# Kernel optimization log

Hardware: AMD Instinct MI355X
Metric: run time of the kernel (lower is better)

Reference implementation:

```python
import jax, jax.numpy as jnp
import numpy as np
from math import factorial, sqrt

# ---------------- irreps utilities ----------------
def parse(s):
    out = []
    for tok in s.split('+'):
        tok = tok.strip()
        mul, ir = (tok.split('x') if 'x' in tok else ('1', tok))
        out.append((int(mul), int(ir[:-1]), 1 if ir[-1] == 'e' else -1))
    return out

def irdim(ir):
    return sum(m * (2 * l + 1) for m, l, p in ir)

def slices(ir):
    s, o = [], 0
    for m, l, p in ir:
        s.append((o, m, l, p)); o += m * (2 * l + 1)
    return s

# ---------------- real Clebsch-Gordan coefficients ----------------
def _cgc(j1, m1, j2, m2, j3, m3):
    if m1 + m2 != m3:
        return 0.0
    f = factorial
    pre = sqrt((2 * j3 + 1) * f(j3 + j1 - j2) * f(j3 - j1 + j2) * f(j1 + j2 - j3) / f(j1 + j2 + j3 + 1))
    pre *= sqrt(f(j3 + m3) * f(j3 - m3) * f(j1 - m1) * f(j1 + m1) * f(j2 - m2) * f(j2 + m2))
    s = 0.0
    for k in range(max(0, j2 - j3 - m1, j1 - j3 + m2), min(j1 + j2 - j3, j1 - m1, j2 + m2) + 1):
        s += (-1) ** k / (f(k) * f(j1 + j2 - j3 - k) * f(j1 - m1 - k) * f(j2 + m2 - k) * f(j3 - j2 + m1 + k) * f(j3 - j1 - m2 + k))
    return pre * s

def _c2r(l):
    # complex -> real spherical-harmonic change of basis
    q = np.zeros((2 * l + 1, 2 * l + 1), dtype=complex); r2 = 1 / np.sqrt(2)
    q[l, l] = 1.0
    for mu in range(1, l + 1):
        q[mu + l, mu + l] = (-1) ** mu * r2; q[mu + l, -mu + l] = r2
        q[-mu + l, -mu + l] = 1j * r2;       q[-mu + l, mu + l] = -1j * (-1) ** mu * r2
    return q

_CGMEM = {}
def cg_real(l1, l2, l3):
    key = (l1, l2, l3)
    if key in _CGMEM:
        return _CGMEM[key]
    C = np.zeros((2 * l1 + 1, 2 * l2 + 1, 2 * l3 + 1))
    for m1 in range(-l1, l1 + 1):
        for m2 in range(-l2, l2 + 1):
            if abs(m1 + m2) <= l3:
                C[m1 + l1, m2 + l2, m1 + m2 + l3] = _cgc(l1, m1, l2, m2, l3, m1 + m2)
    T = np.einsum('am,bn,co,mno->abc', _c2r(l1), _c2r(l2), np.conj(_c2r(l3)), C)
    R = T.real if np.abs(T.real).sum() >= np.abs(T.imag).sum() else T.imag
    _CGMEM[key] = np.ascontiguousarray(R)
    return _CGMEM[key]

# ---------------- equivariant ops ----------------
def tp_paths(ir1, ir2, iro):
    P = []
    for (o1, m1, l1, p1) in slices(ir1):
        for (o2, m2, l2, p2) in slices(ir2):
            for (oo, mo, lo, po) in slices(iro):
                if po == p1 * p2 and abs(l1 - l2) <= lo <= l1 + l2:
                    P.append((o1, m1, l1, o2, m2, l2, oo, mo, lo))
    return P

def tp_numel(P):
    return sum(m1 * m2 * mo for (_, m1, _, _, m2, _, _, mo, _) in P)

def tp_apply(ir1, ir2, iro, x1, x2, w):
    # FullyConnectedTensorProduct with per-row (shared_weights=False) weights w:[E, numel]
    P = tp_paths(ir1, ir2, iro)
    out = jnp.zeros((x1.shape[0], irdim(iro)), x1.dtype)
    fan = {}
    for p in P:
        fan[p[6]] = fan.get(p[6], 0) + p[1] * p[4]
    off = 0
    for (o1, m1, l1, o2, m2, l2, oo, mo, lo) in P:
        cg = jnp.asarray(cg_real(l1, l2, lo), x1.dtype)
        a = x1[:, o1:o1 + m1 * (2 * l1 + 1)].reshape(-1, m1, 2 * l1 + 1)
        b = x2[:, o2:o2 + m2 * (2 * l2 + 1)].reshape(-1, m2, 2 * l2 + 1)
        ww = w[:, off:off + m1 * m2 * mo].reshape(-1, m1, m2, mo); off += m1 * m2 * mo
        r = jnp.einsum('eui,evj,euvw,ijk->ewk', a, b, ww, cg) / np.sqrt(fan[oo])
        out = out.at[:, oo:oo + mo * (2 * lo + 1)].add(r.reshape(-1, mo * (2 * lo + 1)))
    return out

def lin_pairs(iri, iro):
    return [(si, so) for si in slices(iri) for so in slices(iro) if si[2] == so[2] and si[3] == so[3]]

def lin_numel(iri, iro):
    return sum(si[1] * so[1] for si, so in lin_pairs(iri, iro))

def lin_apply(iri, iro, x, w):
    # o3.Linear: per-irrep channel mixing with fan-in normalization
    out = jnp.zeros((x.shape[0], irdim(iro)), x.dtype)
    pairs = lin_pairs(iri, iro)
    fan = {}
    for si, so in pairs:
        fan[so[0]] = fan.get(so[0], 0) + si[1]
    off = 0
    for (oi, mi, li, pi), (oo, mo, lo, po) in pairs:
        W = w[off:off + mi * mo].reshape(mi, mo); off += mi * mo
        xb = x[:, oi:oi + mi * (2 * li + 1)].reshape(-1, mi, 2 * li + 1)
        r = jnp.einsum('eui,uv->evi', xb, W) / np.sqrt(fan[oo])
        out = out.at[:, oo:oo + mo * (2 * lo + 1)].add(r.reshape(-1, mo * (2 * lo + 1)))
    return out

def act_apply(ir, acts, x):
    # tanh on scalar irreps only (flags in acts), identity elsewhere
    parts = []
    for (o, m, l, p), a in zip(slices(ir), acts):
        b = x[:, o:o + m * (2 * l + 1)]
        parts.append(jnp.tanh(b) if a else b)
    return jnp.concatenate(parts, axis=1)

def fc_apply(x, w, dims):
    # e3nn FullyConnectedNet: relu MLP with 1/sqrt(fan_in) weight normalization
    off, h = 0, x
    for i in range(len(dims) - 1):
        di, do = dims[i], dims[i + 1]
        W = w[off:off + di * do].reshape(di, do); off += di * do
        h = (h @ W) / np.sqrt(di)
        if i < len(dims) - 2:
            h = jax.nn.relu(h)
    return h

# ---------------- module irreps (from V_theta.__init__) ----------------
IRR_IN = parse('2x0e')
IRR_SH = parse('1x0e+1x1o+1x2e')
MID1 = parse('8x0e+8x1o+8x2e')
MID2 = parse('8x0e+8x0o+8x1e+8x1o+8x2e+8x2o')
IRR_HH = parse('4x0e+2x1o+2x1o+1x0e+1x1e+1x2e')
IRR_CC = parse('9x0e+6x1o+3x2e+6x1o+' + '1x0e+1x1e+1x2e+' * 4 + '1x1o+1x2o+1x3o+' * 2 + '3x2e+' + '1x1o+1x2o+1x3o+' * 2 + '1x0e+1x1e+1x2e+1x3e+1x4e')
IRR_CH = parse('6x0e+3x1o+4x1o+' + '1x0e+1x1e+1x2e+' * 2 + '2x2e+1x1o+1x2o+1x3o')
SCR = parse('32x0e+1x2e'); SCR2 = parse('1x0e+1x2e'); G1 = parse('32x0e'); G2 = parse('3x0e')
ACT2 = [1, 0, 0]; ACT3 = [1, 1, 0, 0, 0, 0]
P1 = tp_paths(IRR_IN, IRR_SH, MID1); P2 = tp_paths(MID1, IRR_SH, MID2); PB = tp_paths(MID2, MID2, MID2)
EMB_N = 16
FC1D = [1, EMB_N, EMB_N, EMB_N, tp_numel(P1)]
FC2D = [1, EMB_N, EMB_N, EMB_N, tp_numel(P2)]
FCBD = [1, EMB_N, EMB_N, EMB_N, tp_numel(PB)]

def fcsz(d):
    return sum(d[i] * d[i + 1] for i in range(len(d) - 1))

N_NODES, N_EDGES, N_BOND, SCALING = 10000, 100000, 1000, 0.2


def setup_inputs() -> dict:
    key = jax.random.key(0)
    ks = jax.random.split(key, 32)
    nrm = lambda i, shp: jax.random.normal(ks[i], shp, jnp.float32)
    return {
        'f_in': nrm(0, (N_NODES, 2)),
        'sh': nrm(1, (N_EDGES, 9)),
        'emb': jax.random.uniform(ks[2], (N_EDGES, 1), jnp.float32),
        'num_neighbors': jnp.full((1,), 10.0, jnp.float32),
        'w_lin1': nrm(3, (lin_numel(IRR_IN, IRR_IN),)),
        'w_lin2': nrm(4, (lin_numel(MID1, MID1),)),
        'w_lin3': nrm(5, (lin_numel(MID2, MID2),)),
        'w_linCC': nrm(6, (lin_numel(MID2, IRR_CC),)),
        'w_linHH': nrm(7, (lin_numel(MID2, IRR_HH),)),
        'w_linCH': nrm(8, (lin_numel(MID2, IRR_CH),)),
        'w_linC': nrm(9, (lin_numel(MID2, IRR_CC),)),
        'w_linH': nrm(10, (lin_numel(MID2, IRR_HH),)),
        'w_screen1': nrm(11, (lin_numel(MID2, SCR),)),
        'w_screen2': nrm(12, (lin_numel(SCR, SCR2),)),
        'w_gap1': nrm(13, (lin_numel(MID2, G1),)),
        'w_gap2': nrm(14, (lin_numel(G1, G2),)),
        'w_fc1': nrm(15, (fcsz(FC1D),)),
        'w_fc2': nrm(16, (fcsz(FC2D),)),
        'w_fcb': nrm(17, (fcsz(FCBD),)),
        'edge_src': jax.random.randint(ks[18], (N_EDGES,), 0, N_NODES),
        'edge_dst': jax.random.randint(ks[19], (N_EDGES,), 0, N_NODES),
        'HH_ind': jax.random.randint(ks[20], (N_BOND,), 0, N_EDGES),
        'CC_ind': jax.random.randint(ks[21], (N_BOND,), 0, N_EDGES),
        'CH_ind': jax.random.randint(ks[22], (N_BOND,), 0, N_EDGES),
        'num_nodes': N_NODES,
    }


def reference(f_in, sh, emb, num_neighbors, w_lin1, w_lin2, w_lin3, w_linCC, w_linHH, w_linCH, w_linC, w_linH, w_screen1, w_screen2, w_gap1, w_gap2, w_fc1, w_fc2, w_fcb, edge_src, edge_dst, HH_ind, CC_ind, CH_ind, num_nodes):
    inv = 1.0 / jnp.sqrt(num_neighbors)  # .div(num_neighbors**0.5)
    # layer 1: linear + tanh, gather -> TP with per-edge weights -> scatter-add
    x = jnp.tanh(lin_apply(IRR_IN, IRR_IN, f_in, w_lin1))
    ef = tp_apply(IRR_IN, IRR_SH, MID1, x[edge_src], sh, fc_apply(emb, w_fc1, FC1D))
    x = jax.ops.segment_sum(ef, edge_dst, num_segments=num_nodes) * inv
    x = act_apply(MID1, ACT2, lin_apply(MID1, MID1, x, w_lin2))
    # layer 2
    ef = tp_apply(MID1, IRR_SH, MID2, x[edge_src], sh, fc_apply(emb, w_fc2, FC2D))
    x = jax.ops.segment_sum(ef, edge_dst, num_segments=num_nodes) * inv
    x = act_apply(MID2, ACT3, lin_apply(MID2, MID2, x, w_lin3))
    # bond-level tensor products on edge subsets
    def bond(ind):
        return tp_apply(MID2, MID2, MID2, x[edge_src[ind]], x[edge_dst[ind]], fc_apply(emb[ind], w_fcb, FCBD))
    HHf, CCf, CHf = bond(HH_ind), bond(CC_ind), bond(CH_ind)
    eHH = lin_apply(MID2, IRR_HH, act_apply(MID2, ACT3, HHf), w_linHH)
    eCC = lin_apply(MID2, IRR_CC, act_apply(MID2, ACT3, CCf), w_linCC)
    eCH = lin_apply(MID2, IRR_CH, act_apply(MID2, ACT3, CHf), w_linCH)
    nC = lin_apply(MID2, IRR_CC, x, w_linC)
    nH = lin_apply(MID2, IRR_HH, x, w_linH)
    screen = lin_apply(SCR, SCR2, act_apply(SCR, [1, 0], lin_apply(MID2, SCR, x, w_screen1)), w_screen2)
    def gap(F):
        return lin_apply(G1, G2, jnp.tanh(lin_apply(MID2, G1, F, w_gap1)), w_gap2)
    s = SCALING
    # order: H, C, HH, CH, CC, screen, gap[CC], gap[HH], gap[CH]
    return (nH * s, nC * s, eHH * s, eCH * s, eCC * s, screen, gap(CCf), gap(HHf), gap(CHf))
```

## Files before the change

### kernel.cpp

```cpp
#include <hip/hip_runtime.h>
#include <hip/hip_bf16.h>

typedef __hip_bfloat16 bf16_t;

#define N_NODES 10000
#define N_EDGES 100000
#define N_BONDS 1000
#define RPW 20

__device__ __forceinline__ float bf2f(bf16_t v){ return __bfloat162float(v); }
__device__ __forceinline__ bf16_t f2bf(float v){ return __float2bfloat16(v); }
__device__ __forceinline__ int iabs(int x){ return x<0?-x:x; }

constexpr bool cg_nz(int l1,int l2,int l3,int i,int j,int k){
  int m1=i-l1, m2=j-l2, m3=k-l3;
  int neg=(m1<0)+(m2<0)+(m3<0);
  if (((neg ^ (l1+l2+l3)) & 1)!=0) return false;
  int a1=m1<0?-m1:m1, a2=m2<0?-m2:m2, a3=m3<0?-m3:m3;
  return (a3==a1+a2)||(a3==a1-a2)||(a3==a2-a1);
}

__device__ __forceinline__ void stout(void* out, size_t idx, float v, bool f32o){
  if (f32o) ((float*)out)[idx]=v;
  else      ((bf16_t*)out)[idx]=f2bf(v);
}

__global__ void detect_k(const unsigned short* nnb_raw, int* flag){
  *flag = (nnb_raw[0]==0x4120) ? 0 : 1;
}

struct CvtArgs {
  const void* src[19];
  float* dst[19];
  int n[19];
};

__global__ __launch_bounds__(256) void convert_k(CvtArgs a, const int* flag){
  bool f32 = (*flag)!=0;
  int tid = blockIdx.x*256+threadIdx.x;
  int nth = gridDim.x*256;
  for(int t=0;t<19;++t){
    int n=a.n[t];
    float* d=a.dst[t];
    if (f32){
      const float* s=(const float*)a.src[t];
      for(int i=tid;i<n;i+=nth) d[i]=s[i];
    } else {
      const bf16_t* s=(const bf16_t*)a.src[t];
      for(int i=tid;i<n;i+=nth) d[i]=bf2f(s[i]);
    }
  }
}

__global__ __launch_bounds__(256) void csr_count_k(const int* __restrict__ edst, int* __restrict__ cnt){
  int e=blockIdx.x*256+threadIdx.x; if(e>=N_EDGES) return;
  atomicAdd(&cnt[edst[e]],1);
}

__global__ __launch_bounds__(256) void csr_scan_k(const int* __restrict__ cnt,
    int* __restrict__ rowptr, int* __restrict__ pos){
  __shared__ int ssum[256];
  int t=threadIdx.x;
  int base=t*40;
  int s=0;
  for(int i=0;i<40;++i){ int idx=base+i; s += (idx<N_NODES)? cnt[idx]:0; }
  ssum[t]=s; __syncthreads();
  if(t==0){ int run=0; for(int i=0;i<256;++i){ int v=ssum[i]; ssum[i]=run; run+=v; } }
  __syncthreads();
  int run=ssum[t];
  for(int i=0;i<40;++i){
    int idx=base+i;
    if(idx<N_NODES){ rowptr[idx]=run; pos[idx]=run; run+=cnt[idx]; }
  }
  if(t==255) rowptr[N_NODES]=run;
}

__global__ __launch_bounds__(256) void csr_scatter_k(const int* __restrict__ edst,
    int* __restrict__ pos, int* __restrict__ sorted){
  int e=blockIdx.x*256+threadIdx.x; if(e>=N_EDGES) return;
  int p=atomicAdd(&pos[edst[e]],1);
  sorted[p]=e;
}

__device__ __forceinline__ double dfact(int n){
  const double F[11]={1.,1.,2.,6.,24.,120.,720.,5040.,40320.,362880.,3628800.};
  return F[n];
}

__device__ double cgc_d(int j1,int m1,int j2,int m2,int j3,int m3){
  if (m1+m2!=m3) return 0.0;
  double pre = sqrt((double)(2*j3+1)*dfact(j3+j1-j2)*dfact(j3-j1+j2)*dfact(j1+j2-j3)/dfact(j1+j2+j3+1));
  pre *= sqrt(dfact(j3+m3)*dfact(j3-m3)*dfact(j1-m1)*dfact(j1+m1)*dfact(j2-m2)*dfact(j2+m2));
  int k0 = max(0, max(j2-j3-m1, j1-j3+m2));
  int k1 = min(j1+j2-j3, min(j1-m1, j2+m2));
  double s=0.0;
  for(int k=k0;k<=k1;++k)
    s += ((k&1)?-1.0:1.0)/(dfact(k)*dfact(j1+j2-j3-k)*dfact(j1-m1-k)*dfact(j2+m2-k)*dfact(j3-j2+m1+k)*dfact(j3-j1-m2+k));
  return pre*s;
}

__device__ void c2r_d(int l,int a,int m,double&re,double&im){
  re=0.0; im=0.0;
  const double r2 = 0.7071067811865475244;
  int mu = a-l;
  if (mu==0){ if (m==l) re=1.0; return; }
  if (mu>0){
    if (m==l+mu) re = (mu&1)? -r2 : r2;
    else if (m==l-mu) re = r2;
  } else {
    int nu=-mu;
    if (m==l-nu) im = r2;
    else if (m==l+nu) im = (nu&1)? r2 : -r2;
  }
}

__global__ __launch_bounds__(128) void cg_init_k(float* cg){
  int b=blockIdx.x;
  int l1=b/9, l2=(b/3)%3, l3=b%3;
  if (l3 < iabs(l1-l2) || l3 > l1+l2) return;
  int n1=2*l1+1,n2=2*l2+1,n3=2*l3+1,n=n1*n2*n3;
  __shared__ double sRe[125], sIm[125];
  __shared__ int sPick;
  int t=threadIdx.x;
  if (t<n){
    int a=t/(n2*n3), bb=(t/n3)%n2, c=t%n3;
    double re=0.0, im=0.0;
    for(int m1=0;m1<n1;++m1){
      double q1r,q1i; c2r_d(l1,a,m1,q1r,q1i);
      if (q1r==0.0 && q1i==0.0) continue;
      for(int m2=0;m2<n2;++m2){
        double q2r,q2i; c2r_d(l2,bb,m2,q2r,q2i);
        if (q2r==0.0 && q2i==0.0) continue;
        int m3=(m1-l1)+(m2-l2)+l3;
        if (m3<0||m3>=n3) continue;
        double q3r,q3i; c2r_d(l3,c,m3,q3r,q3i); q3i=-q3i;
        double C = cgc_d(l1,m1-l1,l2,m2-l2,l3,m3-l3);
        if (C==0.0) continue;
        double ar = q1r*q2r - q1i*q2i;
        double ai = q1r*q2i + q1i*q2r;
        re += (ar*q3r - ai*q3i)*C;
        im += (ar*q3i + ai*q3r)*C;
      }
    }
    sRe[t]=re; sIm[t]=im;
  }
  __syncthreads();
  if (t==0){
    double s1=0.0,s2=0.0;
    for(int i=0;i<n;++i){ s1+=fabs(sRe[i]); s2+=fabs(sIm[i]); }
    sPick = (s1>=s2)?1:0;
  }
  __syncthreads();
  if (t<n) cg[b*125+t] = (float)(sPick? sRe[t] : sIm[t]);
}

__global__ __launch_bounds__(256) void nodeA_k(const float* __restrict__ fin,
                                               const float* __restrict__ w,
                                               float* __restrict__ x1){
  int n=blockIdx.x*256+threadIdx.x; if(n>=N_NODES) return;
  float f0=fin[2*n], f1=fin[2*n+1];
  const float r2=0.70710678f;
  x1[2*n]   = tanhf((f0*w[0]+f1*w[2])*r2);
  x1[2*n+1] = tanhf((f0*w[1]+f1*w[3])*r2);
}

__device__ __forceinline__ void mlp16(float e, const float* w, float* h){
  float a[16];
  #pragma unroll
  for(int j=0;j<16;++j) a[j]=fmaxf(e*w[j],0.f);
  float b[16];
  #pragma unroll
  for(int j=0;j<16;++j){
    float s=0.f;
    #pragma unroll
    for(int i=0;i<16;++i) s+=a[i]*w[16+i*16+j];
    b[j]=fmaxf(s*0.25f,0.f);
  }
  #pragma unroll
  for(int j=0;j<16;++j){
    float s=0.f;
    #pragma unroll
    for(int i=0;i<16;++i) s+=b[i]*w[272+i*16+j];
    h[j]=fmaxf(s*0.25f,0.f);
  }
}

__global__ __launch_bounds__(256) void hmlp_k(const float* __restrict__ emb,
    const float* __restrict__ wfc, float* __restrict__ H, int E){
  __shared__ float sw[528];
  for(int t=threadIdx.x;t<528;t+=256) sw[t]=wfc[t];
  __syncthreads();
  int e=blockIdx.x*256+threadIdx.x; if(e>=E) return;
  float h[16]; mlp16(emb[e], sw, h);
  float4* H4=(float4*)(H+(size_t)e*16);
  #pragma unroll
  for(int q=0;q<4;++q) H4[q]=make_float4(h[4*q],h[4*q+1],h[4*q+2],h[4*q+3]);
}

__global__ __launch_bounds__(256) void hb_k(const float* __restrict__ emb,
    const float* __restrict__ wfc, const int* __restrict__ i0,
    const int* __restrict__ i1, const int* __restrict__ i2,
    float* __restrict__ HB){
  __shared__ float sw[528];
  for(int t=threadIdx.x;t<528;t+=256) sw[t]=wfc[t];
  __syncthreads();
  int t=blockIdx.x*256+threadIdx.x; if(t>=3*N_BONDS) return;
  const int* ind = (t<N_BONDS)? i0 : (t<2*N_BONDS? i1 : i2);
  int ie = ind[t%N_BONDS];
  float h[16]; mlp16(emb[ie], sw, h);
  float4* H4=(float4*)(HB+(size_t)t*16);
  #pragma unroll
  for(int q=0;q<4;++q) H4[q]=make_float4(h[4*q],h[4*q+1],h[4*q+2],h[4*q+3]);
}

__global__ __launch_bounds__(256) void gemm16_k(const float* __restrict__ A,
    const float* __restrict__ B, float* __restrict__ C, int Eloc, int N,
    const int* __restrict__ idx){
  __shared__ float As[64][16];
  int tid=threadIdx.x;
  int et=blockIdx.x, ct=blockIdx.y;
  for(int t=tid;t<64*16;t+=256){
    int r=t/16, i=t%16;
    int e=et*64+r;
    int ea=(e<Eloc)? (idx? idx[e]:e) : -1;
    As[r][i]=(ea>=0)? A[(size_t)ea*16+i] : 0.f;
  }
  __syncthreads();
  int col=ct*64+(tid&63);
  int eq=tid>>6;
  bool colok = col<N;
  float Breg[16];
  #pragma unroll
  for(int i=0;i<16;++i) Breg[i]= colok? B[(size_t)i*N+col]*0.25f : 0.f;
  #pragma unroll 4
  for(int es=0;es<16;++es){
    int e=et*64+eq*16+es;
    if (e>=Eloc) break;
    float acc=0.f;
    #pragma unroll
    for(int i=0;i<16;++i) acc+=As[eq*16+es][i]*Breg[i];
    if (colok) C[(size_t)e*N+col]=acc;
  }
}

__global__ __launch_bounds__(256) void edge1b_k(const float* __restrict__ x1,
    const float* __restrict__ sh, const float* __restrict__ ww1,
    const int* __restrict__ esrc, const int* __restrict__ sorted,
    const int* __restrict__ rowptr, const float* __restrict__ nnb,
    float* __restrict__ xout){
  int tid=threadIdx.x;
  int n=blockIdx.x*32 + (tid>>3);
  int w8=tid&7;
  if (n>=N_NODES) return;
  float inv = rsqrtf(nnb[0]);
  const float c = 0.70710678f*inv;
  float acc[9];
  #pragma unroll
  for(int t=0;t<9;++t) acc[t]=0.f;
  int r0=rowptr[n], r1=rowptr[n+1];
  for(int r=r0;r<r1;++r){
    int e=sorted[r];
    int src=esrc[e];
    float a0=x1[2*src], a1=x1[2*src+1];
    const float* wr=ww1+(size_t)r*48;
    float w0=wr[w8],    w1=wr[8+w8];
    float w2=wr[16+w8], w3=wr[24+w8];
    float w4=wr[32+w8], w5=wr[40+w8];
    const float* b=sh+(size_t)e*9;
    float s0=w0*a0+w1*a1;
    acc[0]+=s0*b[0];
    float s1=w2*a0+w3*a1;
    #pragma unroll
    for(int j=0;j<3;++j) acc[1+j]+=s1*b[1+j];
    float s2=w4*a0+w5*a1;
    #pragma unroll
    for(int j=0;j<5;++j) acc[4+j]+=s2*b[4+j];
  }
  float* o=xout+(size_t)n*72;
  o[w8]=acc[0]*c;
  #pragma unroll
  for(int j=0;j<3;++j) o[8+w8*3+j]=acc[1+j]*c;
  #pragma unroll
  for(int j=0;j<5;++j) o[32+w8*5+j]=acc[4+j]*c;
}

__global__ __launch_bounds__(256) void lin2b_k(float* __restrict__ x, const float* __restrict__ w){
  __shared__ float sX[32*72];
  __shared__ float sW[192];
  int tid=threadIdx.x;
  int base=blockIdx.x*32;
  if (tid<192) sW[tid]=w[tid];
  for(int t=tid;t<32*72;t+=256){
    int n=base+t/72;
    sX[t] = (n<N_NODES)? x[(size_t)n*72 + t%72] : 0.f;
  }
  __syncthreads();
  int ns=tid>>3, v=tid&7;
  const float r8=0.35355339f;
  const float* X=sX+ns*72;
  float r[9];
  {
    float a=0.f;
    #pragma unroll
    for(int u=0;u<8;++u) a+=X[u]*sW[u*8+v];
    r[0]=tanhf(a*r8);
  }
  #pragma unroll
  for(int i=0;i<3;++i){
    float a=0.f;
    #pragma unroll
    for(int u=0;u<8;++u) a+=X[8+u*3+i]*sW[64+u*8+v];
    r[1+i]=a*r8;
  }
  #pragma unroll
  for(int i=0;i<5;++i){
    float a=0.f;
    #pragma unroll
    for(int u=0;u<8;++u) a+=X[32+u*5+i]*sW[128+u*8+v];
    r[4+i]=a*r8;
  }
  __syncthreads();
  float* Xw=sX+ns*72;
  Xw[v]=r[0];
  #pragma unroll
  for(int i=0;i<3;++i) Xw[8+v*3+i]=r[1+i];
  #pragma unroll
  for(int i=0;i<5;++i) Xw[32+v*5+i]=r[4+i];
  __syncthreads();
  for(int t=tid;t<32*72;t+=256){
    int n=base+t/72;
    if (n<N_NODES) x[(size_t)n*72 + t%72]=sX[t];
  }
}

__global__ __launch_bounds__(256) void lin3b_k(float* __restrict__ x, const float* __restrict__ w){
  __shared__ float sX[32*144];
  __shared__ float sW[384];
  int tid=threadIdx.x;
  int base=blockIdx.x*32;
  for(int t=tid;t<384;t+=256) sW[t]=w[t];
  for(int t=tid;t<32*144;t+=256){
    int n=base+t/144;
    sX[t] = (n<N_NODES)? x[(size_t)n*144 + t%144] : 0.f;
  }
  __syncthreads();
  int ns=tid>>3, v=tid&7;
  const float r8=0.35355339f;
  const float* X=sX+ns*144;
  float r[18];
  {
    float a=0.f;
    #pragma unroll
    for(int u=0;u<8;++u) a+=X[u]*sW[u*8+v];
    r[0]=tanhf(a*r8);
  }
  {
    float a=0.f;
    #pragma unroll
    for(int u=0;u<8;++u) a+=X[8+u]*sW[64+u*8+v];
    r[1]=tanhf(a*r8);
  }
  #pragma unroll
  for(int i=0;i<3;++i){
    float a=0.f;
    #pragma unroll
    for(int u=0;u<8;++u) a+=X[16+u*3+i]*sW[128+u*8+v];
    r[2+i]=a*r8;
  }
  #pragma unroll
  for(int i=0;i<3;++i){
    float a=0.f;
    #pragma unroll
    for(int u=0;u<8;++u) a+=X[40+u*3+i]*sW[192+u*8+v];
    r[5+i]=a*r8;
  }
  #pragma unroll
  for(int i=0;i<5;++i){
    float a=0.f;
    #pragma unroll
    for(int u=0;u<8;++u) a+=X[64+u*5+i]*sW[256+u*8+v];
    r[8+i]=a*r8;
  }
  #pragma unroll
  for(int i=0;i<5;++i){
    float a=0.f;
    #pragma unroll
    for(int u=0;u<8;++u) a+=X[104+u*5+i]*sW[320+u*8+v];
    r[13+i]=a*r8;
  }
  __syncthreads();
  float* Xw=sX+ns*144;
  Xw[v]=r[0];
  Xw[8+v]=r[1];
  #pragma unroll
  for(int i=0;i<3;++i) Xw[16+v*3+i]=r[2+i];
  #pragma unroll
  for(int i=0;i<3;++i) Xw[40+v*3+i]=r[5+i];
  #pragma unroll
  for(int i=0;i<5;++i) Xw[64+v*5+i]=r[8+i];
  #pragma unroll
  for(int i=0;i<5;++i) Xw[104+v*5+i]=r[13+i];
  __syncthreads();
  for(int t=tid;t<32*144;t+=256){
    int n=base+t/144;
    if (n<N_NODES) x[(size_t)n*144 + t%144]=sX[t];
  }
}

template<int L1,int L2,int LO,int BO,int SLOT>
__device__ __forceinline__ void tp_acc(const float* Au, const float* b,
    const float* __restrict__ cg, float wv, float* acc){
  constexpr int D1=2*L1+1, D2=2*L2+1, DN=2*LO+1;
  const float* C = cg + ((L1*3+L2)*3+LO)*125;
  float P[DN];
  #pragma unroll
  for(int k=0;k<DN;++k) P[k]=0.f;
  #pragma unroll
  for(int i=0;i<D1;++i){
    float av=Au[i];
    #pragma unroll
    for(int j=0;j<D2;++j){
      #pragma unroll
      for(int k=0;k<DN;++k){
        if (cg_nz(L1,L2,LO,i,j,k)){
          float cv=C[(i*D2+j)*DN+k];
          P[k]+=av*(cv*b[BO+j]);
        }
      }
    }
  }
  #pragma unroll
  for(int k=0;k<DN;++k) acc[SLOT+k]+=wv*P[k];
}

__device__ __forceinline__ void e2_finish2(float* acc, float inv, float* __restrict__ o, bool first){
  int lane=threadIdx.x&63;
  int w=lane&7;
  #pragma unroll
  for(int t=0;t<18;++t){
    acc[t]+=__shfl_xor(acc[t],8,64);
    acc[t]+=__shfl_xor(acc[t],16,64);
    acc[t]+=__shfl_xor(acc[t],32,64);
  }
  if (lane<8){
    float f0 =rsqrtf(24.f)*inv;
    float f1e=rsqrtf(16.f)*inv;
    float f1o=rsqrtf(32.f)*inv;
    float f2e=rsqrtf(32.f)*inv;
    float f2o=rsqrtf(16.f)*inv;
    if (first){
      o[0+w]=acc[0]*f0;
      o[8+w]=0.f;
      #pragma unroll
      for(int k=0;k<3;++k) o[16+w*3+k]=acc[2+k]*f1e;
      #pragma unroll
      for(int k=0;k<3;++k) o[40+w*3+k]=acc[5+k]*f1o;
      #pragma unroll
      for(int k=0;k<5;++k) o[64+w*5+k]=acc[8+k]*f2e;
      #pragma unroll
      for(int k=0;k<5;++k) o[104+w*5+k]=acc[13+k]*f2o;
    } else {
      o[0+w]+=acc[0]*f0;
      #pragma unroll
      for(int k=0;k<3;++k) o[16+w*3+k]+=acc[2+k]*f1e;
      #pragma unroll
      for(int k=0;k<3;++k) o[40+w*3+k]+=acc[5+k]*f1o;
      #pragma unroll
      for(int k=0;k<5;++k) o[64+w*5+k]+=acc[8+k]*f2e;
      #pragma unroll
      for(int k=0;k<5;++k) o[104+w*5+k]+=acc[13+k]*f2o;
    }
  }
}

__device__ __forceinline__ void e2_flush(float* acc, float inv, float* __restrict__ o){
  int lane=threadIdx.x&63;
  int w=lane&7;
  #pragma unroll
  for(int t=0;t<18;++t){
    acc[t]+=__shfl_xor(acc[t],8,64);
    acc[t]+=__shfl_xor(acc[t],16,64);
    acc[t]+=__shfl_xor(acc[t],32,64);
  }
  if (lane<8){
    float f0 =rsqrtf(24.f)*inv;
    float f1e=rsqrtf(16.f)*inv;
    float f1o=rsqrtf(32.f)*inv;
    float f2e=rsqrtf(32.f)*inv;
    float f2o=rsqrtf(16.f)*inv;
    atomicAdd(&o[0+w], acc[0]*f0);
    #pragma unroll
    for(int k=0;k<3;++k) atomicAdd(&o[16+w*3+k], acc[2+k]*f1e);
    #pragma unroll
    for(int k=0;k<3;++k) atomicAdd(&o[40+w*3+k], acc[5+k]*f1o);
    #pragma unroll
    for(int k=0;k<5;++k) atomicAdd(&o[64+w*5+k], acc[8+k]*f2e);
    #pragma unroll
    for(int k=0;k<5;++k) atomicAdd(&o[104+w*5+k], acc[13+k]*f2o);
  }
}

__device__ __forceinline__ void e2c_consume(const float* __restrict__ xn,
    const float* __restrict__ sh, const float* __restrict__ cg,
    const float* wwp, int e, int src, int u, int lane, float* acc){
  float sv[15];
  sv[ 0]=wwp[  0+lane]; sv[ 1]=wwp[256+lane]; sv[ 2]=wwp[768+lane];
  sv[ 3]=wwp[320+lane]; sv[ 4]=wwp[832+lane];
  sv[ 5]=wwp[ 64+lane]; sv[ 6]=wwp[192+lane]; sv[ 7]=wwp[448+lane]; sv[ 8]=wwp[640+lane];
  sv[ 9]=wwp[128+lane]; sv[10]=wwp[384+lane]; sv[11]=wwp[576+lane]; sv[12]=wwp[896+lane];
  sv[13]=wwp[512+lane]; sv[14]=wwp[704+lane];
  const float* A = xn + (size_t)src*72;
  float b[9];
  #pragma unroll
  for(int j=0;j<9;++j) b[j]=sh[(size_t)e*9+j];
  float a0[1]; a0[0]=A[u];
  float a1[3];
  #pragma unroll
  for(int i=0;i<3;++i) a1[i]=A[8+u*3+i];
  float a2[5];
  #pragma unroll
  for(int i=0;i<5;++i) a2[i]=A[32+u*5+i];
  tp_acc<0,0,0,0, 0>(a0,b,cg,sv[ 0],acc);
  tp_acc<1,1,0,1, 0>(a1,b,cg,sv[ 1],acc);
  tp_acc<2,2,0,4, 0>(a2,b,cg,sv[ 2],acc);
  tp_acc<1,1,1,1, 2>(a1,b,cg,sv[ 3],acc);
  tp_acc<2,2,1,4, 2>(a2,b,cg,sv[ 4],acc);
  tp_acc<0,1,1,1, 5>(a0,b,cg,sv[ 5],acc);
  tp_acc<1,0,1,0, 5>(a1,b,cg,sv[ 6],acc);
  tp_acc<1,2,1,4, 5>(a1,b,cg,sv[ 7],acc);
  tp_acc<2,1,1,1, 5>(a2,b,cg,sv[ 8],acc);
  tp_acc<0,2,2,4, 8>(a0,b,cg,sv[ 9],acc);
  tp_acc<1,1,2,1, 8>(a1,b,cg,sv[10],acc);
  tp_acc<2,0,2,0, 8>(a2,b,cg,sv[11],acc);
  tp_acc<2,2,2,4, 8>(a2,b,cg,sv[12],acc);
  tp_acc<1,2,2,4,13>(a1,b,cg,sv[13],acc);
  tp_acc<2,1,2,1,13>(a2,b,cg,sv[14],acc);
}

__global__ __launch_bounds__(256) void edge2r_k(const float* __restrict__ xn,
    const float* __restrict__ sh, const float* __restrict__ ww2,
    const int* __restrict__ esrc, const int* __restrict__ sorted,
    const int* __restrict__ rowptr, const float* __restrict__ nnb,
    const float* __restrict__ cg, float* __restrict__ xout,
    int rb, int re){
  int gw=blockIdx.x*4+(threadIdx.x>>6);
  int lane=threadIdx.x&63;
  int u=lane>>3;
  int rs=rb+gw*RPW;
  if (rs>=re) return;
  int rend=min(rs+RPW, re);
  float inv=rsqrtf(nnb[0]);
  int lo=0, hi=N_NODES-1;
  while(lo<hi){ int mid=(lo+hi+1)>>1; if(rowptr[mid]<=rs) lo=mid; else hi=mid-1; }
  int n=lo;
  int nend=rowptr[n+1];
  float acc[18];
  #pragma unroll
  for(int t=0;t<18;++t) acc[t]=0.f;
  bool dirty=false;
  for(int r=rs;r<rend;++r){
    while(r>=nend){
      if (dirty){
        e2_flush(acc, inv, xout+(size_t)n*144);
        #pragma unroll
        for(int t=0;t<18;++t) acc[t]=0.f;
        dirty=false;
      }
      n++; nend=rowptr[n+1];
    }
    int e=__builtin_amdgcn_readfirstlane(sorted[r]);
    int src=__builtin_amdgcn_readfirstlane(esrc[e]);
    e2c_consume(xn,sh,cg, ww2+(size_t)(r-rb)*960, e,src,u,lane,acc);
    dirty=true;
  }
  if (dirty) e2_flush(acc, inv, xout+(size_t)n*144);
}

__global__ __launch_bounds__(256) void edge2c_k(const float* __restrict__ xn,
    const float* __restrict__ sh, const float* __restrict__ h2,
    const float* __restrict__ Wg, const int* __restrict__ esrc,
    const int* __restrict__ sorted, const int* __restrict__ rowptr,
    const float* __restrict__ nnb, const float* __restrict__ cg,
    float* __restrict__ xout){
  __shared__ float ww[2][4][960];
  __shared__ int sE[4];
  __shared__ int sCnt[4];
  int tid=threadIdx.x, wid=tid>>6, lane=tid&63;
  int n=blockIdx.x*4+wid;
  int u=lane>>3;
  float inv=rsqrtf(nnb[0]);
  int r0=rowptr[n], r1=rowptr[n+1];
  if (lane==0) sCnt[wid]=r1-r0;
  __syncthreads();
  int mx = max(max(sCnt[0],sCnt[1]),max(sCnt[2],sCnt[3]));
  float acc[18];
  #pragma unroll
  for(int t=0;t<18;++t) acc[t]=0.f;
  int pe=0, psrc=0; bool pact=false;
  for(int t=0;t<mx;++t){
    int r=r0+t;
    bool act=(r<r1);
    int e=0, src=0;
    if (act){
      e=__builtin_amdgcn_readfirstlane(sorted[r]);
      src=__builtin_amdgcn_readfirstlane(esrc[e]);
    }
    if (lane==0) sE[wid]= act? e : -1;
    __syncthreads();
    if (tid<240){
      int e0=max(sE[0],0), e1=max(sE[1],0), e2i=max(sE[2],0), e3=max(sE[3],0);
      const float* h0=h2+(size_t)e0*16;
      const float* h1=h2+(size_t)e1*16;
      const float* hq=h2+(size_t)e2i*16;
      const float* h3=h2+(size_t)e3*16;
      float4 av[4];
      #pragma unroll
      for(int k=0;k<4;++k) av[k]=make_float4(0.f,0.f,0.f,0.f);
      #pragma unroll
      for(int i=0;i<16;++i){
        float hx=h0[i], hy=h1[i], hz=hq[i], hw=h3[i];
        const float* Wr=Wg+i*960;
        #pragma unroll
        for(int k=0;k<4;++k){
          float w=Wr[tid+240*k];
          av[k].x+=hx*w; av[k].y+=hy*w; av[k].z+=hz*w; av[k].w+=hw*w;
        }
      }
      float* wb=&ww[t&1][0][0];
      #pragma unroll
      for(int k=0;k<4;++k){
        int c=tid+240*k;
        wb[c]=av[k].x*0.25f; wb[960+c]=av[k].y*0.25f;
        wb[1920+c]=av[k].z*0.25f; wb[2880+c]=av[k].w*0.25f;
      }
    }
    if (pact){
      const float* wwp=&ww[(t&1)^1][wid][0];
      e2c_consume(xn,sh,cg,wwp,pe,psrc,u,lane,acc);
    }
    pe=e; psrc=src; pact=act;
    __syncthreads();
  }
  if (pact){
    const float* wwp=&ww[(mx-1)&1][wid][0];
    e2c_consume(xn,sh,cg,wwp,pe,psrc,u,lane,acc);
  }
  e2_finish2(acc, inv, xout+(size_t)n*144, true);
}

struct IrS{ short off,m,l,p; };
__device__ const IrS SL_MID2[6]={{0,8,0,1},{8,8,0,-1},{16,8,1,1},{40,8,1,-1},{64,8,2,1},{104,8,2,-1}};
__device__ const IrS SL_HH[6]={{0,4,0,1},{4,2,1,-1},{10,2,1,-1},{16,1,0,1},{17,1,1,1},{20,1,2,1}};
__device__ const IrS SL_CC[34]={{0,9,0,1},{9,6,1,-1},{27,3,2,1},{42,6,1,-1},
 {60,1,0,1},{61,1,1,1},{64,1,2,1},{69,1,0,1},{70,1,1,1},{73,1,2,1},
 {78,1,0,1},{79,1,1,1},{82,1,2,1},{87,1,0,1},{88,1,1,1},{91,1,2,1},
 {96,1,1,-1},{99,1,2,-1},{104,1,3,-1},{111,1,1,-1},{114,1,2,-1},{119,1,3,-1},
 {126,3,2,1},{141,1,1,-1},{144,1,2,-1},{149,1,3,-1},{156,1,1,-1},{159,1,2,-1},{164,1,3,-1},
 {171,1,0,1},{172,1,1,1},{175,1,2,1},{180,1,3,1},{187,1,4,1}};
__device__ const IrS SL_CH[13]={{0,6,0,1},{6,3,1,-1},{15,4,1,-1},{27,1,0,1},{28,1,1,1},{31,1,2,1},
 {36,1,0,1},{37,1,1,1},{40,1,2,1},{45,2,2,1},{55,1,1,-1},{58,1,2,-1},{63,1,3,-1}};

__device__ void lin_out_r(const float* __restrict__ x, bool act16, const float* __restrict__ w,
                          const IrS* so, int no, void* out, size_t base, bool f32o,
                          float scale, int aBeg, int aEnd, bool zf){
  float tx[16];
  bool need_tx = act16 && (aBeg<2);
  if (need_tx){
    #pragma unroll
    for(int i=0;i<16;++i) tx[i]=tanhf(x[i]);
  }
  if (zf){
    for(int bI=0;bI<no;++bI){
      if (so[bI].l>=3){
        int cnt=so[bI].m*(2*so[bI].l+1);
        for(int t=0;t<cnt;++t) stout(out, base+so[bI].off+t, 0.f, f32o);
      }
    }
  }
  int woff=0;
  float f = 0.35355339f*scale;
  for(int a=0;a<6;++a){
    int la=SL_MID2[a].l, pa=SL_MID2[a].p, oa=SL_MID2[a].off;
    int d=2*la+1;
    bool doit = (a>=aBeg && a<aEnd);
    for(int bI=0;bI<no;++bI){
      if (so[bI].l!=la || so[bI].p!=pa) continue;
      int mo=so[bI].m;
      if (doit){
        for(int v=0;v<mo;++v){
          for(int i=0;i<d;++i){
            float acc=0.f;
            for(int u=0;u<8;++u){
              int idx=oa+u*d+i;
              float xv=(act16 && idx<16)? tx[idx] : x[idx];
              acc+=xv*w[woff+u*mo+v];
            }
            stout(out, base+so[bI].off+v*d+i, acc*f, f32o);
          }
        }
      }
      woff+=8*mo;
    }
  }
}

__global__ __launch_bounds__(256) void node_out_k(const float* __restrict__ x,
    const float* __restrict__ wC, const float* __restrict__ wH,
    const float* __restrict__ ws1, const float* __restrict__ ws2,
    void* out, const int* __restrict__ flag){
  int tid=threadIdx.x;
  int gw=blockIdx.x*4+(tid>>6);
  int lane=tid&63;
  int job=gw&7;
  int n=(gw>>3)*64+lane;
  if (n>=N_NODES) return;
  bool f32o = (*flag)!=0;
  const float* X = x + (size_t)n*144;
  if (job==0){
    lin_out_r(X,false,wH,SL_HH,6, out, (size_t)n*25, f32o, 0.2f, 0,6, true);
  } else if (job==1){
    const float r8=0.35355339f, r32=0.17677670f;
    float t0[32];
    for(int v=0;v<32;++v){
      float acc=0.f;
      #pragma unroll
      for(int u=0;u<8;++u) acc+=X[u]*ws1[u*32+v];
      t0[v]=tanhf(acc*r8);
    }
    float t2[5];
    #pragma unroll
    for(int i=0;i<5;++i){
      float acc=0.f;
      #pragma unroll
      for(int u=0;u<8;++u) acc+=X[64+u*5+i]*ws1[256+u];
      t2[i]=acc*r8;
    }
    size_t sb = 2501000 + (size_t)n*6;
    float acc=0.f;
    for(int v=0;v<32;++v) acc+=t0[v]*ws2[v];
    stout(out, sb, acc*r32, f32o);
    float w2e=ws2[32];
    #pragma unroll
    for(int i=0;i<5;++i) stout(out, sb+1+i, t2[i]*w2e, f32o);
  } else {
    int a=job-2;
    lin_out_r(X,false,wC,SL_CC,34, out, 250000 + (size_t)n*196, f32o, 0.2f,
              a, a+1, a==0);
  }
}

template<int L1,int L2,int LO>
__device__ __forceinline__ void bond_path2(const float* sa,int ao,const float* sb,int bo,
    const float* __restrict__ cg, const float* __restrict__ wwp,
    float invfan, float* sF, int oo, int lane){
  constexpr int D1=2*L1+1, D2=2*L2+1, DN=2*LO+1;
  const float* C = cg + ((L1*3+L2)*3+LO)*125;
  int u=lane>>3, v=lane&7;
  float P[DN];
  #pragma unroll
  for(int k=0;k<DN;++k) P[k]=0.f;
  #pragma unroll
  for(int i=0;i<D1;++i){
    float avv=sa[ao+u*D1+i];
    #pragma unroll
    for(int j=0;j<D2;++j){
      #pragma unroll
      for(int k=0;k<DN;++k){
        if (cg_nz(L1,L2,LO,i,j,k)){
          float cv=C[(i*D2+j)*DN+k];
          P[k]+=(avv*sb[bo+v*D2+j])*cv;
        }
      }
    }
  }
  int v2=u;
  float acc[DN];
  #pragma unroll
  for(int k=0;k<DN;++k) acc[k]=0.f;
  #pragma unroll
  for(int u2=0;u2<8;++u2){
    float ww=wwp[u2*64 + lane];
    int srcl=u2*8+v2;
    #pragma unroll
    for(int k=0;k<DN;++k) acc[k]+=ww*__shfl(P[k],srcl,64);
  }
  #pragma unroll
  for(int k=0;k<DN;++k){
    acc[k]+=__shfl_xor(acc[k],8,64);
    acc[k]+=__shfl_xor(acc[k],16,64);
    acc[k]+=__shfl_xor(acc[k],32,64);
  }
  int w=lane&7;
  if (v2==0){
    #pragma unroll
    for(int k=0;k<DN;++k) sF[oo+w*DN+k]+=acc[k]*invfan;
  }
}

__device__ __forceinline__ void bond_disp(int code, const float* a,int ao,const float* bb,int bo,
    const float* __restrict__ cg, const float* __restrict__ wwp,
    float fv, float* Ff, int oo, int lane){
  switch(code){
    case 0:  bond_path2<0,0,0>(a,ao,bb,bo,cg,wwp,fv,Ff,oo,lane); break;
    case 4:  bond_path2<0,1,1>(a,ao,bb,bo,cg,wwp,fv,Ff,oo,lane); break;
    case 8:  bond_path2<0,2,2>(a,ao,bb,bo,cg,wwp,fv,Ff,oo,lane); break;
    case 10: bond_path2<1,0,1>(a,ao,bb,bo,cg,wwp,fv,Ff,oo,lane); break;
    case 12: bond_path2<1,1,0>(a,ao,bb,bo,cg,wwp,fv,Ff,oo,lane); break;
    case 13: bond_path2<1,1,1>(a,ao,bb,bo,cg,wwp,fv,Ff,oo,lane); break;
    case 14: bond_path2<1,1,2>(a,ao,bb,bo,cg,wwp,fv,Ff,oo,lane); break;
    case 16: bond_path2<1,2,1>(a,ao,bb,bo,cg,wwp,fv,Ff,oo,lane); break;
    case 17: bond_path2<1,2,2>(a,ao,bb,bo,cg,wwp,fv,Ff,oo,lane); break;
    case 20: bond_path2<2,0,2>(a,ao,bb,bo,cg,wwp,fv,Ff,oo,lane); break;
    case 22: bond_path2<2,1,1>(a,ao,bb,bo,cg,wwp,fv,Ff,oo,lane); break;
    case 23: bond_path2<2,1,2>(a,ao,bb,bo,cg,wwp,fv,Ff,oo,lane); break;
    case 24: bond_path2<2,2,0>(a,ao,bb,bo,cg,wwp,fv,Ff,oo,lane); break;
    case 25: bond_path2<2,2,1>(a,ao,bb,bo,cg,wwp,fv,Ff,oo,lane); break;
    case 26: bond_path2<2,2,2>(a,ao,bb,bo,cg,wwp,fv,Ff,oo,lane); break;
  }
}

__global__ __launch_bounds__(256) void bond_tpl_k(const float* __restrict__ xn,
    const float* __restrict__ hb, const float* __restrict__ Wg,
    const int* __restrict__ esrc, const int* __restrict__ edst,
    const int* __restrict__ i0, const int* __restrict__ i1,
    const int* __restrict__ i2, const float* __restrict__ cg,
    float* __restrict__ F0, float* __restrict__ F1, float* __restrict__ F2){
  __shared__ float sA[4][144], sB[4][144], sF[4][144];
  __shared__ float ww[2][2048];
  int tid=threadIdx.x;
  int wid=tid>>6, lane=tid&63;
  int gb=blockIdx.x*4+wid;
  int s=gb/N_BONDS, bi=gb-s*N_BONDS;
  const int* ind=(s==0)?i0:(s==1)?i1:i2;
  float* F=(s==0)?F0:(s==1)?F1:F2;
  int ie=ind[bi];
  int src=esrc[ie], dst=edst[ie];
  for(int t=lane;t<144;t+=64){
    sA[wid][t]=xn[(size_t)src*144+t];
    sB[wid][t]=xn[(size_t)dst*144+t];
    sF[wid][t]=0.f;
  }
  float4 hreg[16];
  {
    size_t hbase=(size_t)blockIdx.x*64;
    #pragma unroll
    for(int i=0;i<16;++i)
      hreg[i]=make_float4(hb[hbase+i],hb[hbase+16+i],hb[hbase+32+i],hb[hbase+48+i]);
  }
  const int SL_L[6]={0,0,1,1,2,2};
  const int SL_P[6]={1,-1,1,-1,1,-1};
  const int SL_O[6]={0,8,16,40,64,104};
  const float fi0=rsqrtf(384.f), fi1=rsqrtf(768.f);
  int pidx=0;
  int pcode=0, pao=0, pbo=0, poo=0; float pfv=0.f;
  for(int s1=0;s1<6;++s1){
    for(int s2=0;s2<6;++s2){
      for(int so=0;so<6;++so){
        int l1=SL_L[s1], l2=SL_L[s2], lo=SL_L[so];
        if (SL_P[so]!=SL_P[s1]*SL_P[s2]) continue;
        if (lo<iabs(l1-l2) || lo>l1+l2) continue;
        {
          const float* Wp = Wg + (size_t)pidx*512;
          float4 a0=make_float4(0.f,0.f,0.f,0.f);
          float4 a1=make_float4(0.f,0.f,0.f,0.f);
          #pragma unroll
          for(int i=0;i<16;++i){
            float w0=Wp[(size_t)i*30720 + tid];
            float w1=Wp[(size_t)i*30720 + tid + 256];
            float4 h=hreg[i];
            a0.x+=h.x*w0; a0.y+=h.y*w0; a0.z+=h.z*w0; a0.w+=h.w*w0;
            a1.x+=h.x*w1; a1.y+=h.y*w1; a1.z+=h.z*w1; a1.w+=h.w*w1;
          }
          float* wb=ww[pidx&1];
          wb[0*512+tid]    =a0.x*0.25f;
          wb[1*512+tid]    =a0.y*0.25f;
          wb[2*512+tid]    =a0.z*0.25f;
          wb[3*512+tid]    =a0.w*0.25f;
          wb[0*512+tid+256]=a1.x*0.25f;
          wb[1*512+tid+256]=a1.y*0.25f;
          wb[2*512+tid+256]=a1.z*0.25f;
          wb[3*512+tid+256]=a1.w*0.25f;
        }
        if (pidx>0){
          const float* wwp = ww[(pidx-1)&1] + wid*512;
          bond_disp(pcode, sA[wid], pao, sB[wid], pbo, cg, wwp, pfv, sF[wid], poo, lane);
        }
        pcode=l1*9+l2*3+lo; pao=SL_O[s1]; pbo=SL_O[s2]; poo=SL_O[so];
        pfv=(lo==0)? fi0 : fi1;
        pidx++;
        __syncthreads();
      }
    }
  }
  {
    const float* wwp = ww[(pidx-1)&1] + wid*512;
    bond_disp(pcode, sA[wid], pao, sB[wid], pbo, cg, wwp, pfv, sF[wid], poo, lane);
  }
  __syncthreads();
  for(int t=lane;t<144;t+=64) F[(size_t)bi*144+t]=sF[wid][t];
}

__global__ __launch_bounds__(256) void bond_out_k(const float* __restrict__ F,
    const float* __restrict__ wlin, int tbl, void* out, size_t baseE,
    const float* __restrict__ wg1, const float* __restrict__ wg2,
    size_t baseG, const int* __restrict__ flag){
  int tid=threadIdx.x;
  int gw=blockIdx.x*4+(tid>>6);
  int lane=tid&63;
  int job=gw&7;
  int n=(gw>>3)*64+lane;
  if (n>=N_BONDS) return;
  bool f32o = (*flag)!=0;
  const float* X=F+(size_t)n*144;
  if (job==0){
    const float r8=0.35355339f, r32=0.17677670f;
    float g[32];
    for(int v=0;v<32;++v){
      float acc=0.f;
      #pragma unroll
      for(int u=0;u<8;++u) acc+=X[u]*wg1[u*32+v];
      g[v]=tanhf(acc*r8);
    }
    #pragma unroll
    for(int c=0;c<3;++c){
      float acc=0.f;
      for(int v=0;v<32;++v) acc+=g[v]*wg2[v*3+c];
      stout(out, baseG+(size_t)n*3+c, acc*r32, f32o);
    }
  } else if (job>=2){
    const IrS* so; int no; int dim;
    if(tbl==0){so=SL_HH;no=6;dim=25;}
    else if(tbl==1){so=SL_CC;no=34;dim=196;}
    else {so=SL_CH;no=13;dim=70;}
    int a=job-2;
    lin_out_r(X,true,wlin,so,no,out,baseE+(size_t)n*dim,f32o,0.2f,
              a, a+1, a==0);
  }
}

extern "C" void kernel_launch(void* const* d_in, const int* in_sizes, int n_in,
                              void* d_out, int out_size, void* d_ws, size_t ws_size,
                              hipStream_t stream){
  const int* esrc=(const int*)d_in[19];
  const int* edst=(const int*)d_in[20];
  const int* iHH =(const int*)d_in[21];
  const int* iCC =(const int*)d_in[22];
  const int* iCH =(const int*)d_in[23];
  float* ws=(float*)d_ws;
  int* flag=(int*)d_ws;

  size_t off=16;
  auto alloc=[&](size_t n){ size_t o=off; off+=(n+15)&~(size_t)15; return o; };
  size_t o_cg = alloc(27*125);
  size_t o_st[19];
  for(int i=0;i<19;++i) o_st[i]=alloc((size_t)in_sizes[i]);
  size_t o_x1  = alloc(20000);
  size_t o_xM1 = alloc(720000);
  size_t o_xM2 = alloc(1440000);
  size_t o_F0  = alloc(144000);
  size_t o_F1  = alloc(144000);
  size_t o_F2  = alloc(144000);
  size_t o_h2  = alloc((size_t)N_EDGES*16);
  size_t o_hb  = alloc((size_t)3*N_BONDS*16);
  size_t o_cnt = alloc(10016);
  size_t o_rp  = alloc(10016);
  size_t o_pos = alloc(10016);
  size_t o_srt = alloc(N_EDGES);
  size_t o_h1  = alloc((size_t)N_EDGES*16);
  size_t o_ww1 = alloc((size_t)N_EDGES*48);
  (void)o_ww1;

  float* cg  = ws+o_cg;
  float* x1  = ws+o_x1;
  float* xM1 = ws+o_xM1;
  float* xM2 = ws+o_xM2;
  float* F0  = ws+o_F0;
  float* F1  = ws+o_F1;
  float* F2  = ws+o_F2;
  float* h1  = ws+o_h1;
  float* h2  = ws+o_h2;
  float* hb  = ws+o_hb;
  float* ww1 = ws+o_ww1;
  int* cnt   = (int*)(ws+o_cnt);
  int* rowptr= (int*)(ws+o_rp);
  int* pos   = (int*)(ws+o_pos);
  int* sorted= (int*)(ws+o_srt);

  size_t totf = ws_size/sizeof(float);
  size_t availf = (totf>o_h1)? totf-o_h1 : 0;
  int CHUNK = (int)((availf/960 < (size_t)N_EDGES)? availf/960 : (size_t)N_EDGES);
  bool use_chunk = (CHUNK >= 2000);
  float* ww2 = ws + o_h1;

  CvtArgs ca;
  for(int i=0;i<19;++i){ ca.src[i]=d_in[i]; ca.dst[i]=ws+o_st[i]; ca.n[i]=in_sizes[i]; }
  const float* f_in   = ws+o_st[0];
  const float* sh     = ws+o_st[1];
  const float* emb    = ws+o_st[2];
  const float* nnb    = ws+o_st[3];
  const float* w_lin1 = ws+o_st[4];
  const float* w_lin2 = ws+o_st[5];
  const float* w_lin3 = ws+o_st[6];
  const float* w_linCC= ws+o_st[7];
  const float* w_linHH= ws+o_st[8];
  const float* w_linCH= ws+o_st[9];
  const float* w_linC = ws+o_st[10];
  const float* w_linH = ws+o_st[11];
  const float* w_s1   = ws+o_st[12];
  const float* w_s2   = ws+o_st[13];
  const float* w_g1   = ws+o_st[14];
  const float* w_g2   = ws+o_st[15];
  const float* w_fc1  = ws+o_st[16];
  const float* w_fc2  = ws+o_st[17];
  const float* w_fcb  = ws+o_st[18];

  detect_k<<<1,1,0,stream>>>((const unsigned short*)d_in[3], flag);
  convert_k<<<512,256,0,stream>>>(ca, flag);
  cg_init_k<<<27,128,0,stream>>>(cg);
  hipMemsetAsync(cnt, 0, 10000*sizeof(int), stream);
  csr_count_k<<<391,256,0,stream>>>(edst, cnt);
  csr_scan_k<<<1,256,0,stream>>>(cnt, rowptr, pos);
  csr_scatter_k<<<391,256,0,stream>>>(edst, pos, sorted);

  nodeA_k<<<40,256,0,stream>>>(f_in,w_lin1,x1);
  hmlp_k<<<391,256,0,stream>>>(emb, w_fc1, h1, N_EDGES);
  hmlp_k<<<391,256,0,stream>>>(emb, w_fc2, h2, N_EDGES);
  hb_k<<<12,256,0,stream>>>(emb, w_fcb, iHH, iCC, iCH, hb);

  gemm16_k<<<dim3(1563,1),256,0,stream>>>(h1, w_fc1+528, ww1, N_EDGES, 48, sorted);
  edge1b_k<<<313,256,0,stream>>>(x1,sh,ww1,esrc,sorted,rowptr,nnb,xM1);
  lin2b_k<<<313,256,0,stream>>>(xM1,w_lin2);

  if (use_chunk){
    hipMemsetAsync(xM2, 0, 1440000*sizeof(float), stream);
    int nch = (N_EDGES + CHUNK - 1)/CHUNK;
    for (int ci=0; ci<nch; ++ci){
      int rb = ci*CHUNK;
      int re = rb+CHUNK; if (re>N_EDGES) re=N_EDGES;
      int Cc = re-rb;
      gemm16_k<<<dim3((Cc+63)/64,15),256,0,stream>>>(h2, w_fc2+528, ww2, Cc, 960, sorted+rb);
      int waves=(Cc+RPW-1)/RPW;
      int blocks=(waves+3)/4;
      edge2r_k<<<blocks,256,0,stream>>>(xM1, sh, ww2, esrc, sorted, rowptr,
          nnb, cg, xM2, rb, re);
    }
  } else {
    edge2c_k<<<2500,256,0,stream>>>(xM1, sh, h2, w_fc2+528,
        esrc, sorted, rowptr, nnb, cg, xM2);
  }
  lin3b_k<<<313,256,0,stream>>>(xM2,w_lin3);
  node_out_k<<<314,256,0,stream>>>(xM2,w_linC,w_linH,w_s1,w_s2,d_out,flag);

  bond_tpl_k<<<750,256,0,stream>>>(xM2, hb, w_fcb+528,
      esrc, edst, iHH, iCC, iCH, cg, F0, F1, F2);

  bond_out_k<<<32,256,0,stream>>>(F0,w_linHH,0,d_out,2210000,w_g1,w_g2,2564000,flag);
  bond_out_k<<<32,256,0,stream>>>(F1,w_linCC,1,d_out,2305000,w_g1,w_g2,2561000,flag);
  bond_out_k<<<32,256,0,stream>>>(F2,w_linCH,2,d_out,2235000,w_g1,w_g2,2567000,flag);
}
```

Baseline: 886.1 us.

## Shrink rows per wave, vectorize bond weight loads, fuse bond output launches

Lowers RPW from 20 to 4, so the layer-2 edge kernel launches more waves with fewer CSR rows each, which should improve load balance. Loads and stores the per-bond generated weights as float2 in bond_tpl_k. Merges the three bond_out_k launches into one 96-block kernel that picks its table from blockIdx. Reorders workspace so the chunked ww2 buffer starts at x1 and reuses the x1/F0-F2 region, allowing larger chunks and fewer chunk iterations. The risk is that ww2 aliases buffers that may still be live, and that smaller RPW adds per-wave overhead.

```diff
diff --git a/kernel.cpp b/kernel.cpp
--- a/kernel.cpp
+++ b/kernel.cpp
@@ -6,7 +6,7 @@
 #define N_NODES 10000
 #define N_EDGES 100000
 #define N_BONDS 1000
-#define RPW 20
+#define RPW 4
 
 __device__ __forceinline__ float bf2f(bf16_t v){ return __bfloat162float(v); }
 __device__ __forceinline__ bf16_t f2bf(float v){ return __float2bfloat16(v); }
@@ -860,26 +860,22 @@
         if (SL_P[so]!=SL_P[s1]*SL_P[s2]) continue;
         if (lo<iabs(l1-l2) || lo>l1+l2) continue;
         {
-          const float* Wp = Wg + (size_t)pidx*512;
+          const float* Wp = Wg + (size_t)pidx*512 + 2*tid;
           float4 a0=make_float4(0.f,0.f,0.f,0.f);
           float4 a1=make_float4(0.f,0.f,0.f,0.f);
           #pragma unroll
           for(int i=0;i<16;++i){
-            float w0=Wp[(size_t)i*30720 + tid];
-            float w1=Wp[(size_t)i*30720 + tid + 256];
+            float2 wv = *(const float2*)(Wp + (size_t)i*30720);
             float4 h=hreg[i];
-            a0.x+=h.x*w0; a0.y+=h.y*w0; a0.z+=h.z*w0; a0.w+=h.w*w0;
-            a1.x+=h.x*w1; a1.y+=h.y*w1; a1.z+=h.z*w1; a1.w+=h.w*w1;
+            a0.x+=h.x*wv.x; a0.y+=h.y*wv.x; a0.z+=h.z*wv.x; a0.w+=h.w*wv.x;
+            a1.x+=h.x*wv.y; a1.y+=h.y*wv.y; a1.z+=h.z*wv.y; a1.w+=h.w*wv.y;
           }
           float* wb=ww[pidx&1];
-          wb[0*512+tid]    =a0.x*0.25f;
-          wb[1*512+tid]    =a0.y*0.25f;
-          wb[2*512+tid]    =a0.z*0.25f;
-          wb[3*512+tid]    =a0.w*0.25f;
-          wb[0*512+tid+256]=a1.x*0.25f;
-          wb[1*512+tid+256]=a1.y*0.25f;
-          wb[2*512+tid+256]=a1.z*0.25f;
-          wb[3*512+tid+256]=a1.w*0.25f;
+          int c=2*tid;
+          *(float2*)(wb+0*512+c)=make_float2(a0.x*0.25f, a1.x*0.25f);
+          *(float2*)(wb+1*512+c)=make_float2(a0.y*0.25f, a1.y*0.25f);
+          *(float2*)(wb+2*512+c)=make_float2(a0.z*0.25f, a1.z*0.25f);
+          *(float2*)(wb+3*512+c)=make_float2(a0.w*0.25f, a1.w*0.25f);
         }
         if (pidx>0){
           const float* wwp = ww[(pidx-1)&1] + wid*512;
@@ -900,17 +896,26 @@
   for(int t=lane;t<144;t+=64) F[(size_t)bi*144+t]=sF[wid][t];
 }
 
-__global__ __launch_bounds__(256) void bond_out_k(const float* __restrict__ F,
-    const float* __restrict__ wlin, int tbl, void* out, size_t baseE,
+__global__ __launch_bounds__(256) void bond_out3_k(
+    const float* __restrict__ F0, const float* __restrict__ F1,
+    const float* __restrict__ F2,
+    const float* __restrict__ wHH, const float* __restrict__ wCC,
+    const float* __restrict__ wCH,
     const float* __restrict__ wg1, const float* __restrict__ wg2,
-    size_t baseG, const int* __restrict__ flag){
+    void* out, const int* __restrict__ flag){
+  int tbl=blockIdx.x>>5;
+  int blk=blockIdx.x&31;
   int tid=threadIdx.x;
-  int gw=blockIdx.x*4+(tid>>6);
+  int gw=blk*4+(tid>>6);
   int lane=tid&63;
   int job=gw&7;
   int n=(gw>>3)*64+lane;
   if (n>=N_BONDS) return;
   bool f32o = (*flag)!=0;
+  const float* F = (tbl==0)?F0:(tbl==1)?F1:F2;
+  const float* wlin = (tbl==0)?wHH:(tbl==1)?wCC:wCH;
+  size_t baseE = (tbl==0)?2210000u:(tbl==1)?2305000u:2235000u;
+  size_t baseG = (tbl==0)?2564000u:(tbl==1)?2561000u:2567000u;
   const float* X=F+(size_t)n*144;
   if (job==0){
     const float r8=0.35355339f, r32=0.17677670f;
@@ -954,18 +959,18 @@
   size_t o_cg = alloc(27*125);
   size_t o_st[19];
   for(int i=0;i<19;++i) o_st[i]=alloc((size_t)in_sizes[i]);
-  size_t o_x1  = alloc(20000);
   size_t o_xM1 = alloc(720000);
   size_t o_xM2 = alloc(1440000);
-  size_t o_F0  = alloc(144000);
-  size_t o_F1  = alloc(144000);
-  size_t o_F2  = alloc(144000);
   size_t o_h2  = alloc((size_t)N_EDGES*16);
   size_t o_hb  = alloc((size_t)3*N_BONDS*16);
   size_t o_cnt = alloc(10016);
   size_t o_rp  = alloc(10016);
   size_t o_pos = alloc(10016);
   size_t o_srt = alloc(N_EDGES);
+  size_t o_x1  = alloc(20000);
+  size_t o_F0  = alloc(144000);
+  size_t o_F1  = alloc(144000);
+  size_t o_F2  = alloc(144000);
   size_t o_h1  = alloc((size_t)N_EDGES*16);
   size_t o_ww1 = alloc((size_t)N_EDGES*48);
   (void)o_ww1;
@@ -987,10 +992,10 @@
   int* sorted= (int*)(ws+o_srt);
 
   size_t totf = ws_size/sizeof(float);
-  size_t availf = (totf>o_h1)? totf-o_h1 : 0;
+  size_t availf = (totf>o_x1)? totf-o_x1 : 0;
   int CHUNK = (int)((availf/960 < (size_t)N_EDGES)? availf/960 : (size_t)N_EDGES);
   bool use_chunk = (CHUNK >= 2000);
-  float* ww2 = ws + o_h1;
+  float* ww2 = ws + o_x1;
 
   CvtArgs ca;
   for(int i=0;i<19;++i){ ca.src[i]=d_in[i]; ca.dst[i]=ws+o_st[i]; ca.n[i]=in_sizes[i]; }
@@ -1054,7 +1059,6 @@
   bond_tpl_k<<<750,256,0,stream>>>(xM2, hb, w_fcb+528,
       esrc, edst, iHH, iCC, iCH, cg, F0, F1, F2);
 
-  bond_out_k<<<32,256,0,stream>>>(F0,w_linHH,0,d_out,2210000,w_g1,w_g2,2564000,flag);
-  bond_out_k<<<32,256,0,stream>>>(F1,w_linCC,1,d_out,2305000,w_g1,w_g2,2561000,flag);
-  bond_out_k<<<32,256,0,stream>>>(F2,w_linCH,2,d_out,2235000,w_g1,w_g2,2567000,flag);
-}
+  bond_out3_k<<<96,256,0,stream>>>(F0,F1,F2,w_linHH,w_linCC,w_linCH,
+      w_g1,w_g2,d_out,flag);
+}
```

After: 875.4 us. About the same (-1.2%).
